# Kernel tuning notes

Hardware: AMD Instinct MI355X
Metric: run time of the kernel (lower is better)

The kernel has to match this reference:

```python
import jax, jax.numpy as jnp
import numpy as np

E = 1024; H = 16; D = E // H; MAX_LEN = 512; B = 4; N = 1024
EPS = 1e-5
NEG_INF = float('-inf')


def layernorm(x, g, b):
    mu = jnp.mean(x, axis=-1, keepdims=True)
    var = jnp.mean((x - mu) ** 2, axis=-1, keepdims=True)
    return (x - mu) * jax.lax.rsqrt(var + EPS) * g + b


def rel_bias(seq_len, rel_pos):
    # rel_pos: (H, MAX_LEN). bias[h,i,j] = rel_pos[h, i-j] if 0<=i-j<MAX_LEN else -inf
    pos = jnp.arange(seq_len)
    rel = pos[:, None] - pos[None, :]                     # (N, N)
    valid = (rel >= 0) & (rel < rel_pos.shape[-1])
    idx = jnp.clip(rel, 0, rel_pos.shape[-1] - 1)
    gathered = rel_pos[:, idx]                            # (H, N, N)
    return jnp.where(valid[None], gathered, NEG_INF)


def setup_inputs() -> dict:
    key = jax.random.key(0)
    ks = jax.random.split(key, 12)
    s = 0.02
    return {
        'x': jax.random.normal(ks[0], (B, N, E), jnp.float32),
        'rel_pos': jax.random.normal(ks[1], (H, MAX_LEN), jnp.float32),
        'in_proj_w': jax.random.normal(ks[2], (3 * E, E), jnp.float32) * s,
        'in_proj_b': jnp.zeros((3 * E,), jnp.float32),
        'out_w': jax.random.normal(ks[3], (E, E), jnp.float32) * s,
        'out_b': jnp.zeros((E,), jnp.float32),
        'w1': jax.random.normal(ks[4], (4 * E, E), jnp.float32) * s,
        'b1': jnp.zeros((4 * E,), jnp.float32),
        'w2': jax.random.normal(ks[5], (E, 4 * E), jnp.float32) * s,
        'b2': jnp.zeros((E,), jnp.float32),
        'ln1_g': jnp.ones((E,), jnp.float32),
        'ln1_b': jnp.zeros((E,), jnp.float32),
        'ln2_g': jnp.ones((E,), jnp.float32),
        'ln2_b': jnp.zeros((E,), jnp.float32),
    }


def reference(x, rel_pos, in_proj_w, in_proj_b, out_w, out_b,
              w1, b1, w2, b2, ln1_g, ln1_b, ln2_g, ln2_b):
    b, n, e = x.shape
    xn = layernorm(x, ln1_g, ln1_b)
    qkv = xn @ in_proj_w.T + in_proj_b                    # (B, N, 3E)
    q, k, v = jnp.split(qkv, 3, axis=-1)
    # (B, N, E) -> (B, H, N, D)
    def heads(t):
        return t.reshape(b, n, H, D).transpose(0, 2, 1, 3)
    q, k, v = heads(q), heads(k), heads(v)
    bias = rel_bias(n, rel_pos)                           # (H, N, N)
    scores = jnp.einsum('bhnd,bhmd->bhnm', q, k) / np.sqrt(D) + bias[None]
    attn = jax.nn.softmax(scores, axis=-1)
    o = jnp.einsum('bhnm,bhmd->bhnd', attn, v)            # (B, H, N, D)
    o = o.transpose(0, 2, 1, 3).reshape(b, n, e)
    x = x + o @ out_w.T + out_b
    xm = layernorm(x, ln2_g, ln2_b)
    h = jax.nn.relu(xm @ w1.T + b1)
    return x + h @ w2.T + b2
```

## Files before the change

### kernel.cpp

```cpp
#include <hip/hip_runtime.h>
#include <math.h>

#define BB 4
#define NN 1024
#define EE 1024
#define HH 16
#define DD 64
#define MAXLEN 512
#define EPS 1e-5f

typedef __attribute__((ext_vector_type(8))) __bf16 bf16x8;
typedef __attribute__((ext_vector_type(4))) float floatx4;
typedef __attribute__((ext_vector_type(8))) unsigned short ushort8;

__device__ __forceinline__ unsigned short f2bf(float f) {
    unsigned u = __float_as_uint(f);
    u += 0x7fffu + ((u >> 16) & 1u);
    return (unsigned short)(u >> 16);
}
__device__ __forceinline__ float bf2f(unsigned short h) {
    return __uint_as_float(((unsigned)h) << 16);
}

__global__ __launch_bounds__(256) void f2bf_kernel(const float* __restrict__ in,
                                                   unsigned short* __restrict__ out,
                                                   int n4) {
    int i = blockIdx.x * 256 + threadIdx.x;
    if (i < n4) {
        float4 v = ((const float4*)in)[i];
        ushort4 o;
        o.x = f2bf(v.x); o.y = f2bf(v.y); o.z = f2bf(v.z); o.w = f2bf(v.w);
        ((ushort4*)out)[i] = o;
    }
}

__global__ __launch_bounds__(256) void ln_kernel(const float* __restrict__ x,
                                                 const float* __restrict__ g,
                                                 const float* __restrict__ b,
                                                 unsigned short* __restrict__ out) {
    const int row = blockIdx.x;
    const float* xr = x + (size_t)row * EE;
    float s = 0.f, s2 = 0.f;
    for (int j = threadIdx.x; j < EE; j += 256) {
        float v = xr[j];
        s += v; s2 += v * v;
    }
    for (int off = 32; off > 0; off >>= 1) {
        s  += __shfl_xor(s, off);
        s2 += __shfl_xor(s2, off);
    }
    __shared__ float red[8];
    const int wave = threadIdx.x >> 6, lane = threadIdx.x & 63;
    if (lane == 0) { red[wave] = s; red[4 + wave] = s2; }
    __syncthreads();
    s  = red[0] + red[1] + red[2] + red[3];
    s2 = red[4] + red[5] + red[6] + red[7];
    const float mu  = s * (1.0f / EE);
    const float var = s2 * (1.0f / EE) - mu * mu;
    const float inv = rsqrtf(var + EPS);
    unsigned short* orow = out + (size_t)row * EE;
    for (int j = threadIdx.x; j < EE; j += 256) {
        orow[j] = f2bf((xr[j] - mu) * inv * g[j] + b[j]);
    }
}

template <int TN, bool RELU, bool HAS_RES, bool OUT_BF16>
__global__ __launch_bounds__(256) void gemm_bf16_kernel(
    const unsigned short* __restrict__ A,
    const unsigned short* __restrict__ W,
    const float* __restrict__ bias,
    const float* res, void* Cout, int M, int Nc, int K) {
    constexpr int WN = TN / 2;
    constexpr int NJ = WN / 16;
    constexpr int BI = TN / 64;
    __shared__ unsigned short As[2][128 * 32];
    __shared__ unsigned short Bs[2][TN * 32];

    const int tid  = threadIdx.x;
    const int lane = tid & 63;
    const int wv   = tid >> 6;
    const int row0 = blockIdx.y * 128;
    const int col0 = blockIdx.x * TN;
    const int waveM = (wv & 1) * 64;
    const int waveN = (wv >> 1) * WN;

    floatx4 acc[4][NJ];
#pragma unroll
    for (int i = 0; i < 4; ++i)
#pragma unroll
        for (int j = 0; j < NJ; ++j) acc[i][j] = (floatx4){0.f, 0.f, 0.f, 0.f};

    const int lrow = lane >> 2;
    const int lk8  = (lane & 3) * 8;
    const int frow = lane & 15;
    const int kc8  = (lane >> 4) * 8;

    for (int k0 = 0; k0 < K; k0 += 64) {
#pragma unroll
        for (int s = 0; s < 2; ++s) {
            const int kk = k0 + s * 32;
#pragma unroll
            for (int q = 0; q < 2; ++q) {
                const int r = wv * 32 + q * 16;
                const unsigned short* ga = A + (size_t)(row0 + r + lrow) * K + kk + lk8;
                __builtin_amdgcn_global_load_lds(
                    (const __attribute__((address_space(1))) unsigned int*)ga,
                    (__attribute__((address_space(3))) unsigned int*)&As[s][r * 32], 16, 0, 0);
            }
#pragma unroll
            for (int q = 0; q < BI; ++q) {
                const int r = wv * (16 * BI) + q * 16;
                const unsigned short* gb = W + (size_t)(col0 + r + lrow) * K + kk + lk8;
                __builtin_amdgcn_global_load_lds(
                    (const __attribute__((address_space(1))) unsigned int*)gb,
                    (__attribute__((address_space(3))) unsigned int*)&Bs[s][r * 32], 16, 0, 0);
            }
        }
        __syncthreads();

#pragma unroll
        for (int s = 0; s < 2; ++s) {
            bf16x8 af[4], bfr[NJ];
#pragma unroll
            for (int t = 0; t < 4; ++t)
                af[t] = *(const bf16x8*)&As[s][(waveM + t * 16 + frow) * 32 + kc8];
#pragma unroll
            for (int t = 0; t < NJ; ++t)
                bfr[t] = *(const bf16x8*)&Bs[s][(waveN + t * 16 + frow) * 32 + kc8];
#pragma unroll
            for (int i = 0; i < 4; ++i)
#pragma unroll
                for (int j = 0; j < NJ; ++j)
                    acc[i][j] = __builtin_amdgcn_mfma_f32_16x16x32_bf16(
                        af[i], bfr[j], acc[i][j], 0, 0, 0);
        }
        __syncthreads();
    }

    float* Cf = (float*)Cout;
    unsigned short* Cb = (unsigned short*)Cout;
    const int crow = (lane >> 4) * 4;
    const int ccol = lane & 15;
#pragma unroll
    for (int j = 0; j < NJ; ++j) {
        const int n = col0 + waveN + j * 16 + ccol;
        const float bv = bias[n];
#pragma unroll
        for (int i = 0; i < 4; ++i) {
#pragma unroll
            for (int r = 0; r < 4; ++r) {
                const int m = row0 + waveM + i * 16 + crow + r;
                float v = acc[i][j][r] + bv;
                if (HAS_RES) v += res[(size_t)m * Nc + n];
                if (RELU) v = fmaxf(v, 0.f);
                if (OUT_BF16) Cb[(size_t)m * Nc + n] = f2bf(v);
                else          Cf[(size_t)m * Nc + n] = v;
            }
        }
    }
}

__global__ __launch_bounds__(256) void attn_mfma_kernel(
    const unsigned short* __restrict__ qkv,
    const float* __restrict__ rel_pos,
    unsigned short* __restrict__ o) {
    __shared__ unsigned short K_s[2][64][32];
    __shared__ unsigned short V_s[64][72];
    __shared__ unsigned short P_s[4][2][16][32];
    __shared__ float rel_s[MAXLEN];

    const int qt = blockIdx.x, h = blockIdx.y, b = blockIdx.z;
    const int q0 = qt * 64;
    const int tid  = threadIdx.x;
    const int lane = tid & 63;
    const int w    = tid >> 6;
    const int quad = lane >> 4;
    const int c15  = lane & 15;

    rel_s[tid]       = rel_pos[h * MAXLEN + tid];
    rel_s[tid + 256] = rel_pos[h * MAXLEN + tid + 256];

    const size_t rowstride = 3 * EE;
    const size_t base_q = (size_t)(b * NN) * rowstride + h * DD;
    const size_t base_k = base_q + EE;
    const size_t base_v = base_q + 2 * EE;

    bf16x8 aq[2];
    {
        const unsigned short* qrow =
            qkv + base_q + (size_t)(q0 + w * 16 + c15) * rowstride + quad * 8;
        aq[0] = *(const bf16x8*)(qrow);
        aq[1] = *(const bf16x8*)(qrow + 32);
    }

    floatx4 Oacc[4];
#pragma unroll
    for (int j = 0; j < 4; ++j) Oacc[j] = (floatx4){0.f, 0.f, 0.f, 0.f};
    float m_r[4], l_r[4];
#pragma unroll
    for (int r = 0; r < 4; ++r) { m_r[r] = -1e30f; l_r[r] = 0.f; }

    const int jlo = max(0, q0 - (MAXLEN - 1));
    const int c0 = jlo >> 6;
    const int c1 = (q0 + 63) >> 6;

    for (int cc = c0; cc <= c1; ++cc) {
        const int jb0 = cc << 6;
        __syncthreads();

        {
            const int krow = w * 16 + (lane >> 2);
            const int dofs = (lane & 3) * 8;
            const unsigned short* gk =
                qkv + base_k + (size_t)(jb0 + krow) * rowstride + dofs;
            __builtin_amdgcn_global_load_lds(
                (const __attribute__((address_space(1))) unsigned int*)gk,
                (__attribute__((address_space(3))) unsigned int*)&K_s[0][w * 16][0],
                16, 0, 0);
            __builtin_amdgcn_global_load_lds(
                (const __attribute__((address_space(1))) unsigned int*)(gk + 32),
                (__attribute__((address_space(3))) unsigned int*)&K_s[1][w * 16][0],
                16, 0, 0);
        }
        {
            const int key = lane;
            const int d0  = w * 16;
            const unsigned short* gv =
                qkv + base_v + (size_t)(jb0 + key) * rowstride + d0;
            ushort8 va = *(const ushort8*)(gv);
            ushort8 vb = *(const ushort8*)(gv + 8);
#pragma unroll
            for (int ii = 0; ii < 8; ++ii) V_s[d0 + ii][key] = va[ii];
#pragma unroll
            for (int ii = 0; ii < 8; ++ii) V_s[d0 + 8 + ii][key] = vb[ii];
        }
        __syncthreads();

        floatx4 S[4];
#pragma unroll
        for (int jb = 0; jb < 4; ++jb) {
            S[jb] = (floatx4){0.f, 0.f, 0.f, 0.f};
            bf16x8 bk0 = *(const bf16x8*)&K_s[0][jb * 16 + c15][quad * 8];
            bf16x8 bk1 = *(const bf16x8*)&K_s[1][jb * 16 + c15][quad * 8];
            S[jb] = __builtin_amdgcn_mfma_f32_16x16x32_bf16(aq[0], bk0, S[jb], 0, 0, 0);
            S[jb] = __builtin_amdgcn_mfma_f32_16x16x32_bf16(aq[1], bk1, S[jb], 0, 0, 0);
        }

        const int i_base = q0 + w * 16 + quad * 4;
        float sv[4][4];
        float mc[4] = {-1e30f, -1e30f, -1e30f, -1e30f};
#pragma unroll
        for (int jb = 0; jb < 4; ++jb) {
            const int jg = jb0 + jb * 16 + c15;
#pragma unroll
            for (int r = 0; r < 4; ++r) {
                const int rel = (i_base + r) - jg;
                float s;
                if (rel >= 0 && rel < MAXLEN) s = S[jb][r] * 0.125f + rel_s[rel];
                else                          s = -1e30f;
                sv[jb][r] = s;
                mc[r] = fmaxf(mc[r], s);
            }
        }
#pragma unroll
        for (int off = 1; off < 16; off <<= 1)
#pragma unroll
            for (int r = 0; r < 4; ++r) mc[r] = fmaxf(mc[r], __shfl_xor(mc[r], off));

        float alpha[4], psum[4];
#pragma unroll
        for (int r = 0; r < 4; ++r) {
            const float mn = fmaxf(m_r[r], mc[r]);
            alpha[r] = __expf(m_r[r] - mn);
            m_r[r] = mn;
            psum[r] = 0.f;
        }
#pragma unroll
        for (int jb = 0; jb < 4; ++jb)
#pragma unroll
            for (int r = 0; r < 4; ++r) {
                const float p = __expf(sv[jb][r] - m_r[r]);
                sv[jb][r] = p;
                psum[r] += p;
            }
#pragma unroll
        for (int off = 1; off < 16; off <<= 1)
#pragma unroll
            for (int r = 0; r < 4; ++r) psum[r] += __shfl_xor(psum[r], off);
#pragma unroll
        for (int r = 0; r < 4; ++r) l_r[r] = l_r[r] * alpha[r] + psum[r];
#pragma unroll
        for (int jb = 0; jb < 4; ++jb)
#pragma unroll
            for (int r = 0; r < 4; ++r) Oacc[jb][r] *= alpha[r];

#pragma unroll
        for (int jb = 0; jb < 4; ++jb)
#pragma unroll
            for (int r = 0; r < 4; ++r)
                P_s[w][jb >> 1][quad * 4 + r][(jb & 1) * 16 + c15] = f2bf(sv[jb][r]);

        bf16x8 ap0 = *(const bf16x8*)&P_s[w][0][c15][quad * 8];
        bf16x8 ap1 = *(const bf16x8*)&P_s[w][1][c15][quad * 8];

#pragma unroll
        for (int jd = 0; jd < 4; ++jd) {
            bf16x8 bv0 = *(const bf16x8*)&V_s[jd * 16 + c15][quad * 8];
            bf16x8 bv1 = *(const bf16x8*)&V_s[jd * 16 + c15][32 + quad * 8];
            Oacc[jd] = __builtin_amdgcn_mfma_f32_16x16x32_bf16(ap0, bv0, Oacc[jd], 0, 0, 0);
            Oacc[jd] = __builtin_amdgcn_mfma_f32_16x16x32_bf16(ap1, bv1, Oacc[jd], 0, 0, 0);
        }
    }

    float inv[4];
#pragma unroll
    for (int r = 0; r < 4; ++r) inv[r] = 1.0f / l_r[r];
#pragma unroll
    for (int jd = 0; jd < 4; ++jd) {
#pragma unroll
        for (int r = 0; r < 4; ++r) {
            const int row = q0 + w * 16 + quad * 4 + r;
            const int col = h * DD + jd * 16 + c15;
            o[(size_t)(b * NN + row) * EE + col] = f2bf(Oacc[jd][r] * inv[r]);
        }
    }
}

extern "C" void kernel_launch(void* const* d_in, const int* in_sizes, int n_in,
                              void* d_out, int out_size, void* d_ws, size_t ws_size,
                              hipStream_t stream) {
    const float* x         = (const float*)d_in[0];
    const float* rel_pos   = (const float*)d_in[1];
    const float* in_proj_w = (const float*)d_in[2];
    const float* in_proj_b = (const float*)d_in[3];
    const float* out_w     = (const float*)d_in[4];
    const float* out_b     = (const float*)d_in[5];
    const float* w1        = (const float*)d_in[6];
    const float* b1        = (const float*)d_in[7];
    const float* w2        = (const float*)d_in[8];
    const float* b2        = (const float*)d_in[9];
    const float* ln1_g     = (const float*)d_in[10];
    const float* ln1_b     = (const float*)d_in[11];
    const float* ln2_g     = (const float*)d_in[12];
    const float* ln2_b     = (const float*)d_in[13];
    float* out = (float*)d_out;

    char* wsb = (char*)d_ws;
    const size_t MB = 1024 * 1024;
    unsigned short* wqkv_b = (unsigned short*)(wsb + 0);
    unsigned short* wout_b = (unsigned short*)(wsb + 6 * MB);
    unsigned short* w1_b   = (unsigned short*)(wsb + 8 * MB);
    unsigned short* w2_b   = (unsigned short*)(wsb + 16 * MB);
    unsigned short* xn_b   = (unsigned short*)(wsb + 24 * MB);
    unsigned short* qkv_b  = (unsigned short*)(wsb + 32 * MB);
    unsigned short* h_b    = (unsigned short*)(wsb + 32 * MB);
    unsigned short* o_b    = (unsigned short*)(wsb + 56 * MB);

    const int Mrows = BB * NN;

    f2bf_kernel<<<(3 * EE * EE / 4 + 255) / 256, 256, 0, stream>>>(in_proj_w, wqkv_b, 3 * EE * EE / 4);
    f2bf_kernel<<<(EE * EE / 4 + 255) / 256, 256, 0, stream>>>(out_w, wout_b, EE * EE / 4);
    f2bf_kernel<<<(4 * EE * EE / 4 + 255) / 256, 256, 0, stream>>>(w1, w1_b, 4 * EE * EE / 4);
    f2bf_kernel<<<(4 * EE * EE / 4 + 255) / 256, 256, 0, stream>>>(w2, w2_b, 4 * EE * EE / 4);

    ln_kernel<<<Mrows, 256, 0, stream>>>(x, ln1_g, ln1_b, xn_b);
    gemm_bf16_kernel<128, false, false, true><<<dim3(3072 / 128, Mrows / 128), 256, 0, stream>>>(
        xn_b, wqkv_b, in_proj_b, nullptr, qkv_b, Mrows, 3 * EE, EE);
    attn_mfma_kernel<<<dim3(NN / 64, HH, BB), 256, 0, stream>>>(qkv_b, rel_pos, o_b);
    gemm_bf16_kernel<64, false, true, false><<<dim3(EE / 64, Mrows / 128), 256, 0, stream>>>(
        o_b, wout_b, out_b, x, out, Mrows, EE, EE);
    ln_kernel<<<Mrows, 256, 0, stream>>>(out, ln2_g, ln2_b, xn_b);
    gemm_bf16_kernel<128, true, false, true><<<dim3(4 * EE / 128, Mrows / 128), 256, 0, stream>>>(
        xn_b, w1_b, b1, nullptr, h_b, Mrows, 4 * EE, EE);
    gemm_bf16_kernel<64, false, true, false><<<dim3(EE / 64, Mrows / 128), 256, 0, stream>>>(
        h_b, w2_b, b2, out, out, Mrows, EE, 4 * EE);
}
```

Baseline: 376.1 us.

## Split-K the output and FFN-down GEMMs with atomic accumulation into preinitialized output

The two fp32-output GEMMs (attention out-projection and FFN down-projection) now split K across two blocks along grid z and add their partial sums into the output with float atomics. A small kernel first writes residual plus bias into the output buffer. The aim is to double the block count for these narrow GEMMs (256 blocks before) so the GPU's compute units are better filled. The cost is an extra elementwise pass, atomic traffic, and a summation order that is no longer deterministic.

```diff
diff --git a/kernel.cpp b/kernel.cpp
--- a/kernel.cpp
+++ b/kernel.cpp
@@ -32,6 +32,17 @@
         o.x = f2bf(v.x); o.y = f2bf(v.y); o.z = f2bf(v.z); o.w = f2bf(v.w);
         ((ushort4*)out)[i] = o;
     }
+}
+
+__global__ __launch_bounds__(256) void initbias_kernel(const float* __restrict__ res,
+                                                       const float* __restrict__ bias,
+                                                       float* __restrict__ out, int Nc) {
+    int i = blockIdx.x * 256 + threadIdx.x;
+    float4 r = ((const float4*)res)[i];
+    int n0 = (i * 4) & (Nc - 1);
+    float4 bv = *(const float4*)&bias[n0];
+    float4 o = {r.x + bv.x, r.y + bv.y, r.z + bv.z, r.w + bv.w};
+    ((float4*)out)[i] = o;
 }
 
 __global__ __launch_bounds__(256) void ln_kernel(const float* __restrict__ x,
@@ -64,12 +75,12 @@
     }
 }
 
-template <int TN, bool RELU, bool HAS_RES, bool OUT_BF16>
+template <int TN, bool RELU>
 __global__ __launch_bounds__(256) void gemm_bf16_kernel(
     const unsigned short* __restrict__ A,
     const unsigned short* __restrict__ W,
     const float* __restrict__ bias,
-    const float* res, void* Cout, int M, int Nc, int K) {
+    unsigned short* __restrict__ C, int M, int Nc, int K) {
     constexpr int WN = TN / 2;
     constexpr int NJ = WN / 16;
     constexpr int BI = TN / 64;
@@ -137,8 +148,6 @@
         __syncthreads();
     }
 
-    float* Cf = (float*)Cout;
-    unsigned short* Cb = (unsigned short*)Cout;
     const int crow = (lane >> 4) * 4;
     const int ccol = lane & 15;
 #pragma unroll
@@ -151,10 +160,97 @@
             for (int r = 0; r < 4; ++r) {
                 const int m = row0 + waveM + i * 16 + crow + r;
                 float v = acc[i][j][r] + bv;
-                if (HAS_RES) v += res[(size_t)m * Nc + n];
                 if (RELU) v = fmaxf(v, 0.f);
-                if (OUT_BF16) Cb[(size_t)m * Nc + n] = f2bf(v);
-                else          Cf[(size_t)m * Nc + n] = v;
+                C[(size_t)m * Nc + n] = f2bf(v);
+            }
+        }
+    }
+}
+
+template <int TN>
+__global__ __launch_bounds__(256) void gemm_splitk_kernel(
+    const unsigned short* __restrict__ A,
+    const unsigned short* __restrict__ W,
+    float* __restrict__ C, int M, int Nc, int K, int KS) {
+    constexpr int WN = TN / 2;
+    constexpr int NJ = WN / 16;
+    constexpr int BI = TN / 64;
+    __shared__ unsigned short As[2][128 * 32];
+    __shared__ unsigned short Bs[2][TN * 32];
+
+    const int tid  = threadIdx.x;
+    const int lane = tid & 63;
+    const int wv   = tid >> 6;
+    const int row0 = blockIdx.y * 128;
+    const int col0 = blockIdx.x * TN;
+    const int kbase = blockIdx.z * KS;
+    const int waveM = (wv & 1) * 64;
+    const int waveN = (wv >> 1) * WN;
+
+    floatx4 acc[4][NJ];
+#pragma unroll
+    for (int i = 0; i < 4; ++i)
+#pragma unroll
+        for (int j = 0; j < NJ; ++j) acc[i][j] = (floatx4){0.f, 0.f, 0.f, 0.f};
+
+    const int lrow = lane >> 2;
+    const int lk8  = (lane & 3) * 8;
+    const int frow = lane & 15;
+    const int kc8  = (lane >> 4) * 8;
+
+    for (int k0 = kbase; k0 < kbase + KS; k0 += 64) {
+#pragma unroll
+        for (int s = 0; s < 2; ++s) {
+            const int kk = k0 + s * 32;
+#pragma unroll
+            for (int q = 0; q < 2; ++q) {
+                const int r = wv * 32 + q * 16;
+                const unsigned short* ga = A + (size_t)(row0 + r + lrow) * K + kk + lk8;
+                __builtin_amdgcn_global_load_lds(
+                    (const __attribute__((address_space(1))) unsigned int*)ga,
+                    (__attribute__((address_space(3))) unsigned int*)&As[s][r * 32], 16, 0, 0);
+            }
+#pragma unroll
+            for (int q = 0; q < BI; ++q) {
+                const int r = wv * (16 * BI) + q * 16;
+                const unsigned short* gb = W + (size_t)(col0 + r + lrow) * K + kk + lk8;
+                __builtin_amdgcn_global_load_lds(
+                    (const __attribute__((address_space(1))) unsigned int*)gb,
+                    (__attribute__((address_space(3))) unsigned int*)&Bs[s][r * 32], 16, 0, 0);
+            }
+        }
+        __syncthreads();
+
+#pragma unroll
+        for (int s = 0; s < 2; ++s) {
+            bf16x8 af[4], bfr[NJ];
+#pragma unroll
+            for (int t = 0; t < 4; ++t)
+                af[t] = *(const bf16x8*)&As[s][(waveM + t * 16 + frow) * 32 + kc8];
+#pragma unroll
+            for (int t = 0; t < NJ; ++t)
+                bfr[t] = *(const bf16x8*)&Bs[s][(waveN + t * 16 + frow) * 32 + kc8];
+#pragma unroll
+            for (int i = 0; i < 4; ++i)
+#pragma unroll
+                for (int j = 0; j < NJ; ++j)
+                    acc[i][j] = __builtin_amdgcn_mfma_f32_16x16x32_bf16(
+                        af[i], bfr[j], acc[i][j], 0, 0, 0);
+        }
+        __syncthreads();
+    }
+
+    const int crow = (lane >> 4) * 4;
+    const int ccol = lane & 15;
+#pragma unroll
+    for (int j = 0; j < NJ; ++j) {
+        const int n = col0 + waveN + j * 16 + ccol;
+#pragma unroll
+        for (int i = 0; i < 4; ++i) {
+#pragma unroll
+            for (int r = 0; r < 4; ++r) {
+                const int m = row0 + waveM + i * 16 + crow + r;
+                atomicAdd(&C[(size_t)m * Nc + n], acc[i][j][r]);
             }
         }
     }
@@ -357,6 +453,7 @@
     unsigned short* o_b    = (unsigned short*)(wsb + 56 * MB);
 
     const int Mrows = BB * NN;
+    const int N4out = Mrows * EE / 4 / 256;
 
     f2bf_kernel<<<(3 * EE * EE / 4 + 255) / 256, 256, 0, stream>>>(in_proj_w, wqkv_b, 3 * EE * EE / 4);
     f2bf_kernel<<<(EE * EE / 4 + 255) / 256, 256, 0, stream>>>(out_w, wout_b, EE * EE / 4);
@@ -364,14 +461,16 @@
     f2bf_kernel<<<(4 * EE * EE / 4 + 255) / 256, 256, 0, stream>>>(w2, w2_b, 4 * EE * EE / 4);
 
     ln_kernel<<<Mrows, 256, 0, stream>>>(x, ln1_g, ln1_b, xn_b);
-    gemm_bf16_kernel<128, false, false, true><<<dim3(3072 / 128, Mrows / 128), 256, 0, stream>>>(
-        xn_b, wqkv_b, in_proj_b, nullptr, qkv_b, Mrows, 3 * EE, EE);
+    gemm_bf16_kernel<128, false><<<dim3(3072 / 128, Mrows / 128), 256, 0, stream>>>(
+        xn_b, wqkv_b, in_proj_b, qkv_b, Mrows, 3 * EE, EE);
     attn_mfma_kernel<<<dim3(NN / 64, HH, BB), 256, 0, stream>>>(qkv_b, rel_pos, o_b);
-    gemm_bf16_kernel<64, false, true, false><<<dim3(EE / 64, Mrows / 128), 256, 0, stream>>>(
-        o_b, wout_b, out_b, x, out, Mrows, EE, EE);
+    initbias_kernel<<<N4out, 256, 0, stream>>>(x, out_b, out, EE);
+    gemm_splitk_kernel<64><<<dim3(EE / 64, Mrows / 128, 2), 256, 0, stream>>>(
+        o_b, wout_b, out, Mrows, EE, EE, EE / 2);
     ln_kernel<<<Mrows, 256, 0, stream>>>(out, ln2_g, ln2_b, xn_b);
-    gemm_bf16_kernel<128, true, false, true><<<dim3(4 * EE / 128, Mrows / 128), 256, 0, stream>>>(
-        xn_b, w1_b, b1, nullptr, h_b, Mrows, 4 * EE, EE);
-    gemm_bf16_kernel<64, false, true, false><<<dim3(EE / 64, Mrows / 128), 256, 0, stream>>>(
-        h_b, w2_b, b2, out, out, Mrows, EE, 4 * EE);
-}
+    gemm_bf16_kernel<128, true><<<dim3(4 * EE / 128, Mrows / 128), 256, 0, stream>>>(
+        xn_b, w1_b, b1, h_b, Mrows, 4 * EE, EE);
+    initbias_kernel<<<N4out, 256, 0, stream>>>(out, b2, out, EE);
+    gemm_splitk_kernel<64><<<dim3(EE / 64, Mrows / 128, 2), 256, 0, stream>>>(
+        h_b, w2_b, out, Mrows, EE, 4 * EE, 2 * EE);
+}
```

Result: slower. 399.6 us (+6.3%).

## Load GEMM weight fragments directly into registers with double buffering

Applied to the files above, without the earlier changes.

The bf16 GEMM no longer stages the weight (B) tile through shared memory. Each wave loads its B fragments straight from global memory into registers, double-buffered one 64-wide K step ahead, while A is still staged via global_load_lds. This removes the LDS traffic and footprint for B and overlaps B loads with MFMA work. In exchange it raises register pressure and makes the B loads strided and uncoalesced, since each lane reads 16 bytes from a different weight row, and waves sharing a column range now read duplicate data.

```diff
diff --git a/kernel.cpp b/kernel.cpp
--- a/kernel.cpp
+++ b/kernel.cpp
@@ -72,9 +72,7 @@
     const float* res, void* Cout, int M, int Nc, int K) {
     constexpr int WN = TN / 2;
     constexpr int NJ = WN / 16;
-    constexpr int BI = TN / 64;
     __shared__ unsigned short As[2][128 * 32];
-    __shared__ unsigned short Bs[2][TN * 32];
 
     const int tid  = threadIdx.x;
     const int lane = tid & 63;
@@ -95,45 +93,57 @@
     const int frow = lane & 15;
     const int kc8  = (lane >> 4) * 8;
 
-    for (int k0 = 0; k0 < K; k0 += 64) {
-#pragma unroll
-        for (int s = 0; s < 2; ++s) {
-            const int kk = k0 + s * 32;
+    const unsigned short* wbase = W + (size_t)(col0 + waveN + frow) * K + kc8;
+
+    auto loadB = [&](int kk, bf16x8 (&dst)[2][NJ]) {
+#pragma unroll
+        for (int s = 0; s < 2; ++s)
+#pragma unroll
+            for (int t = 0; t < NJ; ++t)
+                dst[s][t] = *(const bf16x8*)(wbase + (size_t)t * 16 * K + kk + s * 32);
+    };
+    auto stageA = [&](int kk0) {
+#pragma unroll
+        for (int s = 0; s < 2; ++s)
 #pragma unroll
             for (int q = 0; q < 2; ++q) {
                 const int r = wv * 32 + q * 16;
-                const unsigned short* ga = A + (size_t)(row0 + r + lrow) * K + kk + lk8;
+                const unsigned short* ga =
+                    A + (size_t)(row0 + r + lrow) * K + kk0 + s * 32 + lk8;
                 __builtin_amdgcn_global_load_lds(
                     (const __attribute__((address_space(1))) unsigned int*)ga,
-                    (__attribute__((address_space(3))) unsigned int*)&As[s][r * 32], 16, 0, 0);
+                    (__attribute__((address_space(3))) unsigned int*)&As[s][r * 32],
+                    16, 0, 0);
             }
-#pragma unroll
-            for (int q = 0; q < BI; ++q) {
-                const int r = wv * (16 * BI) + q * 16;
-                const unsigned short* gb = W + (size_t)(col0 + r + lrow) * K + kk + lk8;
-                __builtin_amdgcn_global_load_lds(
-                    (const __attribute__((address_space(1))) unsigned int*)gb,
-                    (__attribute__((address_space(3))) unsigned int*)&Bs[s][r * 32], 16, 0, 0);
-            }
-        }
-        __syncthreads();
-
+    };
+    auto compute = [&](bf16x8 (&bfr)[2][NJ]) {
 #pragma unroll
         for (int s = 0; s < 2; ++s) {
-            bf16x8 af[4], bfr[NJ];
+            bf16x8 af[4];
 #pragma unroll
             for (int t = 0; t < 4; ++t)
                 af[t] = *(const bf16x8*)&As[s][(waveM + t * 16 + frow) * 32 + kc8];
 #pragma unroll
-            for (int t = 0; t < NJ; ++t)
-                bfr[t] = *(const bf16x8*)&Bs[s][(waveN + t * 16 + frow) * 32 + kc8];
-#pragma unroll
             for (int i = 0; i < 4; ++i)
 #pragma unroll
                 for (int j = 0; j < NJ; ++j)
                     acc[i][j] = __builtin_amdgcn_mfma_f32_16x16x32_bf16(
-                        af[i], bfr[j], acc[i][j], 0, 0, 0);
-        }
+                        af[i], bfr[s][j], acc[i][j], 0, 0, 0);
+        }
+    };
+
+    bf16x8 b0[2][NJ], b1[2][NJ];
+    loadB(0, b0);
+    for (int k0 = 0; k0 < K; k0 += 128) {
+        stageA(k0);
+        loadB(k0 + 64, b1);
+        __syncthreads();
+        compute(b0);
+        __syncthreads();
+        stageA(k0 + 64);
+        if (k0 + 128 < K) loadB(k0 + 128, b0);
+        __syncthreads();
+        compute(b1);
         __syncthreads();
     }
 
```

Measured after the change: 448.8 us. +19.3%, slower.
